# Kernel optimization log

Hardware: AMD Instinct MI355X
Metric: run time of the kernel (lower is better)

## Reference

```python
import jax, jax.numpy as jnp
import numpy as np

B, S, D, H = 2, 2048, 1024, 16
DH = D // H
SCALE = DH ** -0.5


def setup_inputs() -> dict:
    key = jax.random.key(0)
    ks = jax.random.split(key, 12)
    std = D ** -0.5
    return {
        "Q": jax.random.normal(ks[0], (B, S, D), jnp.float32),
        "K": jax.random.normal(ks[1], (B, S, D), jnp.float32),
        "V": jax.random.normal(ks[2], (B, S, D), jnp.float32),
        "mask": jnp.ones((B, S), jnp.int32),
        "Wq": jax.random.normal(ks[3], (D, D), jnp.float32) * std,
        "bq": jnp.zeros((D,), jnp.float32),
        "Wk": jax.random.normal(ks[4], (D, D), jnp.float32) * std,
        "bk": jnp.zeros((D,), jnp.float32),
        "Wv": jax.random.normal(ks[5], (D, D), jnp.float32) * std,
        "bv": jnp.zeros((D,), jnp.float32),
        "Wo": jax.random.normal(ks[6], (D, D), jnp.float32) * std,
        "bo": jnp.zeros((D,), jnp.float32),
    }


def reference(Q, K, V, mask, Wq, bq, Wk, bk, Wv, bv, Wo, bo):
    b, s, d = Q.shape
    # QKV projections (nn.Linear: x @ W.T + b), split into heads -> [b,h,s,dh]
    q = (Q @ Wq.T + bq).reshape(b, s, H, DH).transpose(0, 2, 1, 3)
    k = (K @ Wk.T + bk).reshape(b, s, H, DH).transpose(0, 2, 1, 3)
    v = (V @ Wv.T + bv).reshape(b, s, H, DH).transpose(0, 2, 1, 3)
    # full O(S^2) score matrix, as in the original (non-flash)
    scores = jnp.einsum("bhqd,bhkd->bhqk", q, k) * SCALE
    # padding mask: [b,1,1,s]
    scores = jnp.where(mask[:, None, None, :] == 0, -jnp.inf, scores)
    # causal mask (causal=True)
    causal = jnp.arange(s)[:, None] >= jnp.arange(s)[None, :]
    scores = jnp.where(causal[None, None], scores, -jnp.inf)
    attn = jax.nn.softmax(scores, axis=-1)
    out = jnp.einsum("bhqk,bhkd->bhqd", attn, v)
    out = out.transpose(0, 2, 1, 3).reshape(b, s, d)
    return out @ Wo.T + bo  # dropout p=0 -> identity
```

## Files before the change

kernel.cpp:

```cpp
#include <hip/hip_runtime.h>
#include <hip/hip_bf16.h>
#include <math.h>

#define Bc  2
#define Sc  2048
#define Dc  1024
#define Hc  16
#define DHc 64
#define SCALE 0.125f

typedef __attribute__((ext_vector_type(8))) short short8;
typedef __attribute__((ext_vector_type(4))) float f32x4;

__device__ inline f32x4 mfma16(short8 a, short8 b, f32x4 c) {
    return __builtin_amdgcn_mfma_f32_16x16x32_bf16(a, b, c, 0, 0, 0);
}

typedef __attribute__((address_space(1))) const unsigned int g_u32;
typedef __attribute__((address_space(3))) unsigned int l_u32;
__device__ inline void gld16(const void* g, void* l) {
    __builtin_amdgcn_global_load_lds((g_u32*)g, (l_u32*)l, 16, 0, 0);
}

__device__ inline short8 cvt8(float4 a, float4 b) {
    union { __hip_bfloat16 h[8]; short8 s; } u;
    u.h[0] = __float2bfloat16(a.x); u.h[1] = __float2bfloat16(a.y);
    u.h[2] = __float2bfloat16(a.z); u.h[3] = __float2bfloat16(a.w);
    u.h[4] = __float2bfloat16(b.x); u.h[5] = __float2bfloat16(b.y);
    u.h[6] = __float2bfloat16(b.z); u.h[7] = __float2bfloat16(b.w);
    return u.s;
}

__global__ __launch_bounds__(256) void castall_k(const float* __restrict__ W0, const float* __restrict__ W1,
                                                 const float* __restrict__ W2, const float* __restrict__ W3,
                                                 const float* __restrict__ I0, const float* __restrict__ I1,
                                                 const float* __restrict__ I2,
                                                 __hip_bfloat16* o0, __hip_bfloat16* o1,
                                                 __hip_bfloat16* o2, __hip_bfloat16* o3,
                                                 __hip_bfloat16* o4, __hip_bfloat16* o5,
                                                 __hip_bfloat16* o6)
{
    const int y = blockIdx.y;
    const float* s; __hip_bfloat16* d; size_t n;
    switch (y) {
        case 0: s = W0; d = o0; n = 1u << 20; break;
        case 1: s = W1; d = o1; n = 1u << 20; break;
        case 2: s = W2; d = o2; n = 1u << 20; break;
        case 3: s = W3; d = o3; n = 1u << 20; break;
        case 4: s = I0; d = o4; n = 1u << 22; break;
        case 5: s = I1; d = o5; n = 1u << 22; break;
        default: s = I2; d = o6; n = 1u << 22; break;
    }
    size_t idx = ((size_t)blockIdx.x * 256 + threadIdx.x) * 8;
    if (idx >= n) return;
    float4 a = *(const float4*)(s + idx);
    float4 b = *(const float4*)(s + idx + 4);
    *(short8*)(d + idx) = cvt8(a, b);
}

__global__ __launch_bounds__(256, 3) void qkv_k(const __hip_bfloat16* __restrict__ Qb,
                                                const __hip_bfloat16* __restrict__ Kb,
                                                const __hip_bfloat16* __restrict__ Vb,
                                                const __hip_bfloat16* __restrict__ Wqb,
                                                const __hip_bfloat16* __restrict__ Wkb,
                                                const __hip_bfloat16* __restrict__ Wvb,
                                                const float* __restrict__ bq, const float* __restrict__ bk,
                                                const float* __restrict__ bv,
                                                __hip_bfloat16* __restrict__ qo, __hip_bfloat16* __restrict__ ko,
                                                __hip_bfloat16* __restrict__ vto)
{
    __shared__ __align__(16) __hip_bfloat16 As[128 * 64];
    __shared__ __align__(16) __hip_bfloat16 Bs[128 * 64];
    const int p   = blockIdx.x >> 8;
    const int blk = blockIdx.x & 255;
    const int bm  = blk & 31, bn = blk >> 5;
    const __hip_bfloat16* A = p == 0 ? Qb : p == 1 ? Kb : Vb;
    const __hip_bfloat16* W = p == 0 ? Wqb : p == 1 ? Wkb : Wvb;
    const float* bias = p == 0 ? bq : p == 1 ? bk : bv;

    const int tid = threadIdx.x, wave = tid >> 6, lane = tid & 63;
    const int quad = lane >> 4, l15 = lane & 15;
    const int wm = wave >> 1, wn = wave & 1;
    const int sw = l15 & 7;

    f32x4 acc[4][4] = {};

#pragma unroll
    for (int i = 0; i < 4; ++i) {
        int c = wave * 64 + i * 256 + lane;
        int row = c >> 3, g = (c & 7) ^ (row & 7);
        gld16(A + (size_t)(bm * 128 + row) * 1024 + g * 8, (char*)As + (size_t)c * 16);
        gld16(W + (size_t)(bn * 128 + row) * 1024 + g * 8, (char*)Bs + (size_t)c * 16);
    }

    for (int kki = 0; kki < 16; ++kki) {
        __syncthreads();

        short8 af[4][2], bf2[4][2];
#pragma unroll
        for (int mi = 0; mi < 4; ++mi)
#pragma unroll
            for (int h = 0; h < 2; ++h)
                af[mi][h] = *(const short8*)((char*)As + (size_t)(wm * 64 + mi * 16 + l15) * 128 +
                                             ((((h << 2) + quad) ^ sw) << 4));
#pragma unroll
        for (int ni = 0; ni < 4; ++ni)
#pragma unroll
            for (int h = 0; h < 2; ++h)
                bf2[ni][h] = *(const short8*)((char*)Bs + (size_t)(wn * 64 + ni * 16 + l15) * 128 +
                                              ((((h << 2) + quad) ^ sw) << 4));

        __syncthreads();

        if (kki < 15) {
            const int kk2 = (kki + 1) * 64;
#pragma unroll
            for (int i = 0; i < 4; ++i) {
                int c = wave * 64 + i * 256 + lane;
                int row = c >> 3, g = (c & 7) ^ (row & 7);
                gld16(A + (size_t)(bm * 128 + row) * 1024 + kk2 + g * 8, (char*)As + (size_t)c * 16);
                gld16(W + (size_t)(bn * 128 + row) * 1024 + kk2 + g * 8, (char*)Bs + (size_t)c * 16);
            }
        }

#pragma unroll
        for (int mi = 0; mi < 4; ++mi)
#pragma unroll
            for (int ni = 0; ni < 4; ++ni) {
                acc[mi][ni] = mfma16(af[mi][0], bf2[ni][0], acc[mi][ni]);
                acc[mi][ni] = mfma16(af[mi][1], bf2[ni][1], acc[mi][ni]);
            }
    }

    float bvv[4];
#pragma unroll
    for (int ni = 0; ni < 4; ++ni) bvv[ni] = bias[bn * 128 + wn * 64 + ni * 16 + l15];
#pragma unroll
    for (int mi = 0; mi < 4; ++mi) {
#pragma unroll
        for (int r = 0; r < 4; ++r) {
            int m = bm * 128 + wm * 64 + mi * 16 + quad * 4 + r;
            int b_ = m >> 11, s_ = m & 2047;
#pragma unroll
            for (int ni = 0; ni < 4; ++ni) {
                int n = bn * 128 + wn * 64 + ni * 16 + l15;
                int h_ = n >> 6, d_ = n & 63;
                float val = acc[mi][ni][r] + bvv[ni];
                if (p == 0) val *= SCALE;
                __hip_bfloat16 hv = __float2bfloat16(val);
                if (p < 2) {
                    __hip_bfloat16* dst = (p == 0 ? qo : ko);
                    dst[((size_t)(b_ * Hc + h_) * Sc + s_) * DHc + d_] = hv;
                } else {
                    int loc = s_ & 63;
                    int sp = (s_ & ~63) | ((loc & 15) << 2) | (loc >> 4);
                    vto[((size_t)(b_ * Hc + h_) * DHc + d_) * Sc + sp] = hv;
                }
            }
        }
    }
}

__global__ __launch_bounds__(256, 2) void attn_k(const __hip_bfloat16* __restrict__ qb,
                                                 const __hip_bfloat16* __restrict__ kb,
                                                 const __hip_bfloat16* __restrict__ vtb,
                                                 const int* __restrict__ mask,
                                                 __hip_bfloat16* __restrict__ ob)
{
    __shared__ __align__(16) __hip_bfloat16 Klds[2][64 * 64];
    __shared__ __align__(16) __hip_bfloat16 Vlds[2][64 * 64];
    __shared__ __align__(16) __hip_bfloat16 Plds[4][32 * 72];

    const int qt = 15 - (blockIdx.x >> 5);
    const int bh = blockIdx.x & 31;
    const int b  = bh >> 4;
    const int tid = threadIdx.x, wave = tid >> 6, lane = tid & 63;
    const int quad = lane >> 4, l15 = lane & 15;
    const int sw = l15 & 7;
    const int r0 = qt * 128 + wave * 32;

    const __hip_bfloat16* qh  = qb  + (size_t)bh * Sc * DHc;
    const __hip_bfloat16* kh  = kb  + (size_t)bh * Sc * DHc;
    const __hip_bfloat16* vth = vtb + (size_t)bh * DHc * Sc;

    short8 qf[2][2];
#pragma unroll
    for (int rc = 0; rc < 2; ++rc)
#pragma unroll
        for (int h = 0; h < 2; ++h)
            qf[rc][h] = *(const short8*)(qh + (size_t)(r0 + rc * 16 + l15) * DHc + h * 32 + quad * 8);

    f32x4 O[2][4] = {};
    float lsum[2][4] = {};

    const int nkt = 2 * qt + 2;

#pragma unroll
    for (int i = 0; i < 2; ++i) {
        int c = i * 256 + wave * 64 + lane;
        int row = c >> 3, g = (c & 7) ^ (row & 7);
        gld16(kh + (size_t)row * DHc + g * 8, (char*)&Klds[0][0] + (size_t)c * 16);
        gld16(vth + (size_t)row * Sc + g * 8, (char*)&Vlds[0][0] + (size_t)c * 16);
    }

    for (int kt = 0; kt < nkt; ++kt) {
        __syncthreads();
        if (kt + 1 < nkt) {
            const int kv1 = (kt + 1) * 64, nb = (kt + 1) & 1;
#pragma unroll
            for (int i = 0; i < 2; ++i) {
                int c = i * 256 + wave * 64 + lane;
                int row = c >> 3, g = (c & 7) ^ (row & 7);
                gld16(kh + (size_t)(kv1 + row) * DHc + g * 8, (char*)&Klds[nb][0] + (size_t)c * 16);
                gld16(vth + (size_t)row * Sc + kv1 + g * 8, (char*)&Vlds[nb][0] + (size_t)c * 16);
            }
        }
        const int kv0 = kt * 64, buf = kt & 1;
        if (kv0 >= r0 + 32) continue;

        f32x4 sc[2][4] = {};
#pragma unroll
        for (int h = 0; h < 2; ++h)
#pragma unroll
            for (int nc = 0; nc < 4; ++nc) {
                short8 kf = *(const short8*)((char*)&Klds[buf][0] +
                            (size_t)(nc * 16 + l15) * 128 + ((((h << 2) + quad) ^ sw) << 4));
                sc[0][nc] = mfma16(qf[0][h], kf, sc[0][nc]);
                sc[1][nc] = mfma16(qf[1][h], kf, sc[1][nc]);
            }

        float mb[4];
#pragma unroll
        for (int nc = 0; nc < 4; ++nc)
            mb[nc] = mask[b * Sc + kv0 + nc * 16 + l15] ? 0.f : -__builtin_inff();
        const bool notfull = (kv0 + 64 > r0);

#pragma unroll
        for (int rc = 0; rc < 2; ++rc)
#pragma unroll
            for (int r = 0; r < 4; ++r) {
                const int q_idx = r0 + rc * 16 + quad * 4 + r;
                float pv[4], ps = 0.f;
#pragma unroll
                for (int nc = 0; nc < 4; ++nc) {
                    float s = sc[rc][nc][r] + mb[nc];
                    if (notfull) {
                        int key = kv0 + nc * 16 + l15;
                        s = (key <= q_idx) ? s : -__builtin_inff();
                    }
                    s = fminf(s, 30.f);
                    pv[nc] = __expf(s);
                    ps += pv[nc];
                }
                lsum[rc][r] += ps;
                union { __hip_bfloat16 h[4]; unsigned long long u; } pp;
#pragma unroll
                for (int nc = 0; nc < 4; ++nc) pp.h[nc] = __float2bfloat16(pv[nc]);
                *(unsigned long long*)((char*)&Plds[wave][0] +
                    (size_t)(rc * 16 + quad * 4 + r) * 144 + l15 * 8) = pp.u;
            }

#pragma unroll
        for (int h = 0; h < 2; ++h) {
            short8 pf0 = *(const short8*)((char*)&Plds[wave][0] + (size_t)l15 * 144 + h * 64 + quad * 16);
            short8 pf1 = *(const short8*)((char*)&Plds[wave][0] + (size_t)(16 + l15) * 144 + h * 64 + quad * 16);
#pragma unroll
            for (int nc = 0; nc < 4; ++nc) {
                short8 vf = *(const short8*)((char*)&Vlds[buf][0] +
                            (size_t)(nc * 16 + l15) * 128 + ((((h << 2) + quad) ^ sw) << 4));
                O[0][nc] = mfma16(pf0, vf, O[0][nc]);
                O[1][nc] = mfma16(pf1, vf, O[1][nc]);
            }
        }
    }

#pragma unroll
    for (int rc = 0; rc < 2; ++rc)
#pragma unroll
        for (int r = 0; r < 4; ++r) {
            float l = lsum[rc][r];
#pragma unroll
            for (int off = 1; off < 16; off <<= 1) l += __shfl_xor(l, off);
            const float inv = 1.f / l;
            const int q_idx = r0 + rc * 16 + quad * 4 + r;
#pragma unroll
            for (int nc = 0; nc < 4; ++nc)
                ob[((size_t)bh * Sc + q_idx) * DHc + nc * 16 + l15] =
                    __float2bfloat16(O[rc][nc][r] * inv);
        }
}

__global__ __launch_bounds__(256, 4) void out_k(const __hip_bfloat16* __restrict__ Ab,
                                                const __hip_bfloat16* __restrict__ Wb,
                                                const float* __restrict__ bias,
                                                float* __restrict__ outp)
{
    __shared__ __align__(16) __hip_bfloat16 As[128 * 64];
    __shared__ __align__(16) __hip_bfloat16 Bs[64 * 64];
    const int bm = blockIdx.x & 31, bn = blockIdx.x >> 5;
    const int tid = threadIdx.x, wave = tid >> 6, lane = tid & 63;
    const int quad = lane >> 4, l15 = lane & 15;
    const int wm = wave >> 1, wn = wave & 1;
    const int sw = l15 & 7;

    f32x4 acc[4][2] = {};

#pragma unroll
    for (int i = 0; i < 4; ++i) {
        int c = wave * 64 + i * 256 + lane;
        int row = c >> 3, g = (c & 7) ^ (row & 7);
        int m = bm * 128 + row, b_ = m >> 11, s_ = m & 2047;
        gld16(Ab + (((size_t)(b_ * Hc) * Sc + s_) * DHc + g * 8), (char*)As + (size_t)c * 16);
    }
#pragma unroll
    for (int i = 0; i < 2; ++i) {
        int c = wave * 64 + i * 256 + lane;
        int row = c >> 3, g = (c & 7) ^ (row & 7);
        gld16(Wb + (size_t)(bn * 64 + row) * 1024 + g * 8, (char*)Bs + (size_t)c * 16);
    }

    for (int kki = 0; kki < 16; ++kki) {
        __syncthreads();

        short8 af[4][2], bf2[2][2];
#pragma unroll
        for (int mi = 0; mi < 4; ++mi)
#pragma unroll
            for (int h = 0; h < 2; ++h)
                af[mi][h] = *(const short8*)((char*)As + (size_t)(wm * 64 + mi * 16 + l15) * 128 +
                                             ((((h << 2) + quad) ^ sw) << 4));
#pragma unroll
        for (int ni = 0; ni < 2; ++ni)
#pragma unroll
            for (int h = 0; h < 2; ++h)
                bf2[ni][h] = *(const short8*)((char*)Bs + (size_t)(wn * 32 + ni * 16 + l15) * 128 +
                                              ((((h << 2) + quad) ^ sw) << 4));

        __syncthreads();

        if (kki < 15) {
            const int h2 = kki + 1, kk2 = h2 * 64;
#pragma unroll
            for (int i = 0; i < 4; ++i) {
                int c = wave * 64 + i * 256 + lane;
                int row = c >> 3, g = (c & 7) ^ (row & 7);
                int m = bm * 128 + row, b_ = m >> 11, s_ = m & 2047;
                gld16(Ab + (((size_t)(b_ * Hc + h2) * Sc + s_) * DHc + g * 8), (char*)As + (size_t)c * 16);
            }
#pragma unroll
            for (int i = 0; i < 2; ++i) {
                int c = wave * 64 + i * 256 + lane;
                int row = c >> 3, g = (c & 7) ^ (row & 7);
                gld16(Wb + (size_t)(bn * 64 + row) * 1024 + kk2 + g * 8, (char*)Bs + (size_t)c * 16);
            }
        }

#pragma unroll
        for (int mi = 0; mi < 4; ++mi)
#pragma unroll
            for (int ni = 0; ni < 2; ++ni) {
                acc[mi][ni] = mfma16(af[mi][0], bf2[ni][0], acc[mi][ni]);
                acc[mi][ni] = mfma16(af[mi][1], bf2[ni][1], acc[mi][ni]);
            }
    }

    float bvv[2];
#pragma unroll
    for (int ni = 0; ni < 2; ++ni) bvv[ni] = bias[bn * 64 + wn * 32 + ni * 16 + l15];
#pragma unroll
    for (int mi = 0; mi < 4; ++mi)
#pragma unroll
        for (int r = 0; r < 4; ++r) {
            int m = bm * 128 + wm * 64 + mi * 16 + quad * 4 + r;
#pragma unroll
            for (int ni = 0; ni < 2; ++ni) {
                int n = bn * 64 + wn * 32 + ni * 16 + l15;
                outp[(size_t)m * 1024 + n] = acc[mi][ni][r] + bvv[ni];
            }
        }
}

extern "C" void kernel_launch(void* const* d_in, const int* in_sizes, int n_in,
                              void* d_out, int out_size, void* d_ws, size_t ws_size,
                              hipStream_t stream) {
    const float* Q   = (const float*)d_in[0];
    const float* K   = (const float*)d_in[1];
    const float* V   = (const float*)d_in[2];
    const int*  mask = (const int*)d_in[3];
    const float* Wq  = (const float*)d_in[4];
    const float* bq  = (const float*)d_in[5];
    const float* Wk  = (const float*)d_in[6];
    const float* bk  = (const float*)d_in[7];
    const float* Wv  = (const float*)d_in[8];
    const float* bv  = (const float*)d_in[9];
    const float* Wo  = (const float*)d_in[10];
    const float* bo  = (const float*)d_in[11];

    char* ws = (char*)d_ws;
    __hip_bfloat16* wqb = (__hip_bfloat16*)(ws);
    __hip_bfloat16* wkb = (__hip_bfloat16*)(ws + (2u << 20));
    __hip_bfloat16* wvb = (__hip_bfloat16*)(ws + (4u << 20));
    __hip_bfloat16* wob = (__hip_bfloat16*)(ws + (6u << 20));
    __hip_bfloat16* qbuf  = (__hip_bfloat16*)(ws + (8u << 20));
    __hip_bfloat16* kbuf  = (__hip_bfloat16*)(ws + (16u << 20));
    __hip_bfloat16* vtbuf = (__hip_bfloat16*)(ws + (24u << 20));
    __hip_bfloat16* Qbf   = (__hip_bfloat16*)(ws + (32u << 20));
    __hip_bfloat16* Kbf   = (__hip_bfloat16*)(ws + (40u << 20));
    __hip_bfloat16* Vbf   = (__hip_bfloat16*)(ws + (48u << 20));

    castall_k<<<dim3(2048, 7), 256, 0, stream>>>(Wq, Wk, Wv, Wo, Q, K, V,
                                                 wqb, wkb, wvb, wob, Qbf, Kbf, Vbf);
    qkv_k<<<768, 256, 0, stream>>>(Qbf, Kbf, Vbf, wqb, wkb, wvb, bq, bk, bv, qbuf, kbuf, vtbuf);
    attn_k<<<512, 256, 0, stream>>>(qbuf, kbuf, vtbuf, mask, qbuf);
    out_k<<<512, 256, 0, stream>>>(qbuf, wob, bo, (float*)d_out);
}
```

Measured before the change: 230.6 us.

## Split attention KV range across two blocks and combine partial outputs

Each query tile now runs as two blocks: one takes the even KV tiles and the other the odd ones. Each block writes an unnormalized partial output and its row sums, and a new combine kernel adds the two partials and normalizes. This doubles the grid to raise parallelism and occupancy (launch bounds raised to 3). Separately, the score scale now folds in log2(e) so the softmax can use a native exp2, and the causal-mask check is split into separate full and diagonal paths. The cost is an extra kernel launch, an extra round-trip of partial outputs through memory, and bf16 rounding of the unnormalized partials.

```diff
diff --git a/kernel.cpp b/kernel.cpp
--- a/kernel.cpp
+++ b/kernel.cpp
@@ -7,7 +7,7 @@
 #define Dc  1024
 #define Hc  16
 #define DHc 64
-#define SCALE 0.125f
+#define QSCALE 0.1803368801111244f
 
 typedef __attribute__((ext_vector_type(8))) short short8;
 typedef __attribute__((ext_vector_type(4))) float f32x4;
@@ -21,6 +21,8 @@
 __device__ inline void gld16(const void* g, void* l) {
     __builtin_amdgcn_global_load_lds((g_u32*)g, (l_u32*)l, 16, 0, 0);
 }
+
+__device__ inline float fast_exp2(float x) { return __builtin_amdgcn_exp2f(x); }
 
 __device__ inline short8 cvt8(float4 a, float4 b) {
     union { __hip_bfloat16 h[8]; short8 s; } u;
@@ -146,7 +148,7 @@
                 int n = bn * 128 + wn * 64 + ni * 16 + l15;
                 int h_ = n >> 6, d_ = n & 63;
                 float val = acc[mi][ni][r] + bvv[ni];
-                if (p == 0) val *= SCALE;
+                if (p == 0) val *= QSCALE;
                 __hip_bfloat16 hv = __float2bfloat16(val);
                 if (p < 2) {
                     __hip_bfloat16* dst = (p == 0 ? qo : ko);
@@ -161,18 +163,22 @@
     }
 }
 
-__global__ __launch_bounds__(256, 2) void attn_k(const __hip_bfloat16* __restrict__ qb,
+__global__ __launch_bounds__(256, 3) void attn_k(const __hip_bfloat16* __restrict__ qb,
                                                  const __hip_bfloat16* __restrict__ kb,
                                                  const __hip_bfloat16* __restrict__ vtb,
                                                  const int* __restrict__ mask,
-                                                 __hip_bfloat16* __restrict__ ob)
+                                                 __hip_bfloat16* __restrict__ obE,
+                                                 __hip_bfloat16* __restrict__ obO,
+                                                 float* __restrict__ lsE,
+                                                 float* __restrict__ lsO)
 {
     __shared__ __align__(16) __hip_bfloat16 Klds[2][64 * 64];
     __shared__ __align__(16) __hip_bfloat16 Vlds[2][64 * 64];
     __shared__ __align__(16) __hip_bfloat16 Plds[4][32 * 72];
 
-    const int qt = 15 - (blockIdx.x >> 5);
     const int bh = blockIdx.x & 31;
+    const int kp = (blockIdx.x >> 5) & 1;
+    const int qt = 15 - (blockIdx.x >> 6);
     const int b  = bh >> 4;
     const int tid = threadIdx.x, wave = tid >> 6, lane = tid & 63;
     const int quad = lane >> 4, l15 = lane & 15;
@@ -182,6 +188,8 @@
     const __hip_bfloat16* qh  = qb  + (size_t)bh * Sc * DHc;
     const __hip_bfloat16* kh  = kb  + (size_t)bh * Sc * DHc;
     const __hip_bfloat16* vth = vtb + (size_t)bh * DHc * Sc;
+    __hip_bfloat16* obP = kp ? obO : obE;
+    float*           lsP = kp ? lsO : lsE;
 
     short8 qf[2][2];
 #pragma unroll
@@ -193,20 +201,21 @@
     f32x4 O[2][4] = {};
     float lsum[2][4] = {};
 
-    const int nkt = 2 * qt + 2;
-
-#pragma unroll
-    for (int i = 0; i < 2; ++i) {
-        int c = i * 256 + wave * 64 + lane;
-        int row = c >> 3, g = (c & 7) ^ (row & 7);
-        gld16(kh + (size_t)row * DHc + g * 8, (char*)&Klds[0][0] + (size_t)c * 16);
-        gld16(vth + (size_t)row * Sc + g * 8, (char*)&Vlds[0][0] + (size_t)c * 16);
-    }
-
-    for (int kt = 0; kt < nkt; ++kt) {
+    {
+        const int kv = kp * 64;
+#pragma unroll
+        for (int i = 0; i < 2; ++i) {
+            int c = i * 256 + wave * 64 + lane;
+            int row = c >> 3, g = (c & 7) ^ (row & 7);
+            gld16(kh + (size_t)(kv + row) * DHc + g * 8, (char*)&Klds[0][0] + (size_t)c * 16);
+            gld16(vth + (size_t)row * Sc + kv + g * 8, (char*)&Vlds[0][0] + (size_t)c * 16);
+        }
+    }
+
+    for (int j = 0; j <= qt; ++j) {
         __syncthreads();
-        if (kt + 1 < nkt) {
-            const int kv1 = (kt + 1) * 64, nb = (kt + 1) & 1;
+        if (j < qt) {
+            const int kv1 = (kp + 2 * (j + 1)) * 64, nb = (j + 1) & 1;
 #pragma unroll
             for (int i = 0; i < 2; ++i) {
                 int c = i * 256 + wave * 64 + lane;
@@ -215,7 +224,7 @@
                 gld16(vth + (size_t)row * Sc + kv1 + g * 8, (char*)&Vlds[nb][0] + (size_t)c * 16);
             }
         }
-        const int kv0 = kt * 64, buf = kt & 1;
+        const int kv0 = (kp + 2 * j) * 64, buf = j & 1;
         if (kv0 >= r0 + 32) continue;
 
         f32x4 sc[2][4] = {};
@@ -233,32 +242,49 @@
 #pragma unroll
         for (int nc = 0; nc < 4; ++nc)
             mb[nc] = mask[b * Sc + kv0 + nc * 16 + l15] ? 0.f : -__builtin_inff();
-        const bool notfull = (kv0 + 64 > r0);
-
-#pragma unroll
-        for (int rc = 0; rc < 2; ++rc)
-#pragma unroll
-            for (int r = 0; r < 4; ++r) {
-                const int q_idx = r0 + rc * 16 + quad * 4 + r;
-                float pv[4], ps = 0.f;
-#pragma unroll
-                for (int nc = 0; nc < 4; ++nc) {
-                    float s = sc[rc][nc][r] + mb[nc];
-                    if (notfull) {
+
+        if (kv0 + 64 > r0) {
+#pragma unroll
+            for (int rc = 0; rc < 2; ++rc)
+#pragma unroll
+                for (int r = 0; r < 4; ++r) {
+                    const int q_idx = r0 + rc * 16 + quad * 4 + r;
+                    float pv[4], ps = 0.f;
+#pragma unroll
+                    for (int nc = 0; nc < 4; ++nc) {
                         int key = kv0 + nc * 16 + l15;
+                        float s = sc[rc][nc][r] + mb[nc];
                         s = (key <= q_idx) ? s : -__builtin_inff();
+                        pv[nc] = fast_exp2(fminf(s, 43.f));
+                        ps += pv[nc];
                     }
-                    s = fminf(s, 30.f);
-                    pv[nc] = __expf(s);
-                    ps += pv[nc];
+                    lsum[rc][r] += ps;
+                    union { __hip_bfloat16 h[4]; unsigned long long u; } pp;
+#pragma unroll
+                    for (int nc = 0; nc < 4; ++nc) pp.h[nc] = __float2bfloat16(pv[nc]);
+                    *(unsigned long long*)((char*)&Plds[wave][0] +
+                        (size_t)(rc * 16 + quad * 4 + r) * 144 + l15 * 8) = pp.u;
                 }
-                lsum[rc][r] += ps;
-                union { __hip_bfloat16 h[4]; unsigned long long u; } pp;
-#pragma unroll
-                for (int nc = 0; nc < 4; ++nc) pp.h[nc] = __float2bfloat16(pv[nc]);
-                *(unsigned long long*)((char*)&Plds[wave][0] +
-                    (size_t)(rc * 16 + quad * 4 + r) * 144 + l15 * 8) = pp.u;
-            }
+        } else {
+#pragma unroll
+            for (int rc = 0; rc < 2; ++rc)
+#pragma unroll
+                for (int r = 0; r < 4; ++r) {
+                    float pv[4], ps = 0.f;
+#pragma unroll
+                    for (int nc = 0; nc < 4; ++nc) {
+                        float s = sc[rc][nc][r] + mb[nc];
+                        pv[nc] = fast_exp2(fminf(s, 43.f));
+                        ps += pv[nc];
+                    }
+                    lsum[rc][r] += ps;
+                    union { __hip_bfloat16 h[4]; unsigned long long u; } pp;
+#pragma unroll
+                    for (int nc = 0; nc < 4; ++nc) pp.h[nc] = __float2bfloat16(pv[nc]);
+                    *(unsigned long long*)((char*)&Plds[wave][0] +
+                        (size_t)(rc * 16 + quad * 4 + r) * 144 + l15 * 8) = pp.u;
+                }
+        }
 
 #pragma unroll
         for (int h = 0; h < 2; ++h) {
@@ -281,13 +307,31 @@
             float l = lsum[rc][r];
 #pragma unroll
             for (int off = 1; off < 16; off <<= 1) l += __shfl_xor(l, off);
-            const float inv = 1.f / l;
             const int q_idx = r0 + rc * 16 + quad * 4 + r;
+            if (l15 == 0) lsP[(size_t)bh * Sc + q_idx] = l;
 #pragma unroll
             for (int nc = 0; nc < 4; ++nc)
-                ob[((size_t)bh * Sc + q_idx) * DHc + nc * 16 + l15] =
-                    __float2bfloat16(O[rc][nc][r] * inv);
-        }
+                obP[((size_t)bh * Sc + q_idx) * DHc + nc * 16 + l15] =
+                    __float2bfloat16(O[rc][nc][r]);
+        }
+}
+
+__global__ __launch_bounds__(256) void combine_k(const __hip_bfloat16* __restrict__ Oe,
+                                                 const __hip_bfloat16* __restrict__ Oo,
+                                                 const float* __restrict__ le,
+                                                 const float* __restrict__ lo,
+                                                 __hip_bfloat16* __restrict__ out)
+{
+    size_t t = (size_t)blockIdx.x * 256 + threadIdx.x;
+    size_t row = t >> 3;
+    float inv = 1.f / (le[row] + lo[row]);
+    union { short8 s; __hip_bfloat16 h[8]; } ua, ub, uo;
+    ua.s = *(const short8*)(Oe + t * 8);
+    ub.s = *(const short8*)(Oo + t * 8);
+#pragma unroll
+    for (int i = 0; i < 8; ++i)
+        uo.h[i] = __float2bfloat16((__bfloat162float(ua.h[i]) + __bfloat162float(ub.h[i])) * inv);
+    *(short8*)(out + t * 8) = uo.s;
 }
 
 __global__ __launch_bounds__(256, 4) void out_k(const __hip_bfloat16* __restrict__ Ab,
@@ -407,10 +451,15 @@
     __hip_bfloat16* Qbf   = (__hip_bfloat16*)(ws + (32u << 20));
     __hip_bfloat16* Kbf   = (__hip_bfloat16*)(ws + (40u << 20));
     __hip_bfloat16* Vbf   = (__hip_bfloat16*)(ws + (48u << 20));
+    __hip_bfloat16* Oe    = Qbf;
+    __hip_bfloat16* Oo    = Kbf;
+    float* lsE = (float*)(ws + (48u << 20));
+    float* lsO = (float*)(ws + (48u << 20) + (256u << 10));
 
     castall_k<<<dim3(2048, 7), 256, 0, stream>>>(Wq, Wk, Wv, Wo, Q, K, V,
                                                  wqb, wkb, wvb, wob, Qbf, Kbf, Vbf);
     qkv_k<<<768, 256, 0, stream>>>(Qbf, Kbf, Vbf, wqb, wkb, wvb, bq, bk, bv, qbuf, kbuf, vtbuf);
-    attn_k<<<512, 256, 0, stream>>>(qbuf, kbuf, vtbuf, mask, qbuf);
+    attn_k<<<1024, 256, 0, stream>>>(qbuf, kbuf, vtbuf, mask, Oe, Oo, lsE, lsO);
+    combine_k<<<2048, 256, 0, stream>>>(Oe, Oo, lsE, lsO, qbuf);
     out_k<<<512, 256, 0, stream>>>(qbuf, wob, bo, (float*)d_out);
 }
```

Measured after the change: 209.0 us. -9.4%, faster.
